# Kernel optimization log

Measured on AMD Instinct MI355X. Metric: run time of the kernel, lower is better.

Reference implementation:

```python
import jax, jax.numpy as jnp
import numpy as np

H0, H1, NL, B, S = 2048, 1024, 8, 2, 2048

def _linear(x, w, b):
    return jnp.einsum('bsd,od->bso', x, w) + b

def setup_inputs() -> dict:
    key = jax.random.key(0)
    ks = jax.random.split(key, 32)
    d = {
        'z':    jax.random.normal(ks[0], (B, S, H0), jnp.float32),
        'act0': jax.random.normal(ks[1], (B, S, H0), jnp.float32),
        'act1': jax.random.normal(ks[2], (B, S, H0), jnp.float32),
        'attmask': jax.random.randint(ks[3], (B, S), 0, 2, jnp.int32),
        'dproj_w': jax.random.normal(ks[4], (H1, H0), jnp.float32) * 0.02,
        'dproj_b': jnp.zeros((H1,), jnp.float32),
        'uproj_w': jax.random.normal(ks[5], (H0, H1), jnp.float32) * 0.02,
        'uproj_b': jnp.zeros((H0,), jnp.float32),
        'wq_w': jax.random.normal(ks[6], (NL, H1, H1), jnp.float32) * 0.02,
        'wq_b': jnp.zeros((NL, H1), jnp.float32),
        'wk_w': jax.random.normal(ks[7], (NL, H1, H1), jnp.float32) * 0.02,
        'wk_b': jnp.zeros((NL, H1), jnp.float32),
        'wv_w': jax.random.normal(ks[8], (NL, H1, H1), jnp.float32) * 0.02,
        'wv_b': jnp.zeros((NL, H1), jnp.float32),
        'mlp1_w': jax.random.normal(ks[9], (NL, 4 * H1, H1), jnp.float32) * 0.02,
        'mlp1_b': jnp.zeros((NL, 4 * H1), jnp.float32),
        'mlp2_w': jax.random.normal(ks[10], (NL, H1, 4 * H1), jnp.float32) * 0.02,
        'mlp2_b': jnp.zeros((NL, H1), jnp.float32),
    }
    return d

def _ladder_fwd(z, act0, act1, attmask, dproj_w, dproj_b, uproj_w, uproj_b,
                wq_w, wq_b, wk_w, wk_b, wv_w, wv_b,
                mlp1_w, mlp1_b, mlp2_w, mlp2_b):
    seq = z.shape[1]
    scale = 1.0 / jnp.sqrt(jnp.float32(H1))
    causal = jnp.tril(jnp.ones((seq, seq), bool))  # [S,S]
    pad = (attmask != 0)[:, None, :]               # [B,1,S] key padding mask
    neg = jnp.float32(-1e9)

    def ladsatt(i, x):
        Q = _linear(x, wq_w[i], wq_b[i])
        K = _linear(x, wk_w[i], wk_b[i])
        V = _linear(x, wv_w[i], wv_b[i])
        scores = jnp.einsum('bqd,bkd->bqk', Q, K) * scale
        scores = jnp.where(causal[None], scores, neg)
        scores = jnp.where(pad, scores, neg)
        w = jax.nn.softmax(scores, axis=-1)
        return jnp.einsum('bqk,bkd->bqd', w, V)

    def mlp(i, x):
        h = jax.nn.relu(_linear(x, mlp1_w[i], mlp1_b[i]))
        return _linear(h, mlp2_w[i], mlp2_b[i])

    rs = _linear(act0, dproj_w, dproj_b)
    rs = rs + ladsatt(0, rs)
    rs = rs + mlp(0, rs)
    rs = rs + _linear(act1, dproj_w, dproj_b)
    rs = rs + ladsatt(1, rs)
    rs = rs + mlp(1, rs)
    for i in range(2, NL):
        rs = rs + ladsatt(i, rs)
        rs = rs + mlp(i, rs)
    return _linear(rs, uproj_w, uproj_b) + z

def reference(z, act0, act1, attmask, dproj_w, dproj_b, uproj_w, uproj_b,
              wq_w, wq_b, wk_w, wk_b, wv_w, wv_b,
              mlp1_w, mlp1_b, mlp2_w, mlp2_b):
    return _ladder_fwd(z, act0, act1, attmask, dproj_w, dproj_b, uproj_w, uproj_b,
                       wq_w, wq_b, wk_w, wk_b, wv_w, wv_b,
                       mlp1_w, mlp1_b, mlp2_w, mlp2_b)
```

## Files before the change

kernel.cpp:

```cpp
#include <hip/hip_runtime.h>
#include <cstdint>


typedef unsigned short u16;
typedef __attribute__((ext_vector_type(8))) __bf16 bf16x8;
typedef __attribute__((ext_vector_type(4))) float f32x4;

#define DI __device__ __forceinline__

constexpr int BB = 2, SSQ = 2048, HH0 = 2048, HH1 = 1024, NLAY = 8, HH4 = 4096;
constexpr int MM = BB * SSQ;

DI float bf2f(u16 h) {
  union { uint32_t u; float f; } x; x.u = ((uint32_t)h) << 16; return x.f;
}
DI u16 f2bf(float f) {
  union { float f; uint32_t u; } x; x.f = f;
  uint32_t u = x.u;
  return (u16)((u + 0x7fffu + ((u >> 16) & 1u)) >> 16);
}

enum {
  FB_BIAS = 1, FB_RES = 2, FB_RELU = 4, FB_F32 = 8, FB_SPLIT = 16,
  FB_CSKIP = 32, FB_CKLOOP = 64
};

template <int F, int KSP>
__global__ __launch_bounds__(256) void gemm_split(
    const u16* __restrict__ Ah, const u16* __restrict__ Al, long sAz, int lda,
    const u16* __restrict__ Bh, const u16* __restrict__ Bl, long sBz, int ldb,
    const float* __restrict__ bias, const float* __restrict__ resF,
    float* Cf, u16* Ch, u16* Cl, long sCz, int ldc, int K, long pstride) {
  int gx = gridDim.x, gy = gridDim.y, gz = gridDim.z;
  long o = blockIdx.x + (long)gx * (blockIdx.y + (long)gy * blockIdx.z);
  long nwg = (long)gx * gy * gz;
  long cq = nwg >> 3, cr = nwg & 7;
  long xcd = o & 7, cidx = o >> 3;
  long sl = (xcd < cr ? xcd * (cq + 1) : cr * (cq + 1) + (xcd - cr) * cq) + cidx;
  int bx = (int)(sl % gx);
  long tt = sl / gx;
  int by = (int)(tt % gy);
  int bzf = (int)(tt / gy);
  int NB = gz / KSP;
  int bz = bzf % NB;
  int ks = bzf / NB;

  if ((F & FB_CSKIP) && bx > by) return;

  __shared__ __align__(16) u16 Ash[128 * 32];
  __shared__ __align__(16) u16 Asl[128 * 32];
  __shared__ __align__(16) u16 Bsh[128 * 32];
  __shared__ __align__(16) u16 Bsl[128 * 32];

  int tid = threadIdx.x;
  int lane = tid & 63;
  int wave = tid >> 6;
  int wr = (wave >> 1) << 6;
  int wc = (wave & 1) << 6;
  int lrow = lane & 15;
  int kg = lane >> 4;
  int kc8 = (kg ^ ((lrow >> 1) & 3)) << 3;

  const u16* Abh = Ah + (long)bz * sAz + ((long)(by << 7)) * lda;
  const u16* Abl = Al + (long)bz * sAz + ((long)(by << 7)) * lda;
  const u16* Bbh = Bh + (long)bz * sBz + ((long)(bx << 7)) * ldb;
  const u16* Bbl = Bl + (long)bz * sBz + ((long)(bx << 7)) * ldb;

  int nKtot = (F & FB_CKLOOP) ? ((by + 1) << 2) : (K >> 5);
  int kbeg = (KSP > 1) ? (ks * nKtot) / KSP : 0;
  int kend = (KSP > 1) ? ((ks + 1) * nKtot) / KSP : nKtot;

  f32x4 acc[4][4] = {};

  for (int kt = kbeg; kt < kend; ++kt) {
    __syncthreads();
    int k0 = kt << 5;
#pragma unroll
    for (int it = 0; it < 2; ++it) {
      int sidx = (it << 8) + tid;
      int r = sidx >> 2;
      int jsw = (sidx & 3) ^ ((r >> 1) & 3);
      long goff = (long)r * lda + (k0 + (jsw << 3));
      long gofB = (long)r * ldb + (k0 + (jsw << 3));
      int loff = sidx << 3;
      __builtin_amdgcn_global_load_lds(
          (__attribute__((address_space(1))) void*)(Abh + goff),
          (__attribute__((address_space(3))) void*)(&Ash[loff]), 16, 0, 0);
      __builtin_amdgcn_global_load_lds(
          (__attribute__((address_space(1))) void*)(Abl + goff),
          (__attribute__((address_space(3))) void*)(&Asl[loff]), 16, 0, 0);
      __builtin_amdgcn_global_load_lds(
          (__attribute__((address_space(1))) void*)(Bbh + gofB),
          (__attribute__((address_space(3))) void*)(&Bsh[loff]), 16, 0, 0);
      __builtin_amdgcn_global_load_lds(
          (__attribute__((address_space(1))) void*)(Bbl + gofB),
          (__attribute__((address_space(3))) void*)(&Bsl[loff]), 16, 0, 0);
    }
    __syncthreads();

    bf16x8 afh[4], bfh[4], bfl[4];
#pragma unroll
    for (int mi = 0; mi < 4; ++mi)
      afh[mi] = *(const bf16x8*)&Ash[((wr + (mi << 4) + lrow) << 5) + kc8];
#pragma unroll
    for (int ni = 0; ni < 4; ++ni) {
      bfh[ni] = *(const bf16x8*)&Bsh[((wc + (ni << 4) + lrow) << 5) + kc8];
      bfl[ni] = *(const bf16x8*)&Bsl[((wc + (ni << 4) + lrow) << 5) + kc8];
    }
#pragma unroll
    for (int mi = 0; mi < 4; ++mi)
#pragma unroll
      for (int ni = 0; ni < 4; ++ni) {
        acc[mi][ni] = __builtin_amdgcn_mfma_f32_16x16x32_bf16(
            afh[mi], bfh[ni], acc[mi][ni], 0, 0, 0);
        acc[mi][ni] = __builtin_amdgcn_mfma_f32_16x16x32_bf16(
            afh[mi], bfl[ni], acc[mi][ni], 0, 0, 0);
      }
    bf16x8 afl[4];
#pragma unroll
    for (int mi = 0; mi < 4; ++mi)
      afl[mi] = *(const bf16x8*)&Asl[((wr + (mi << 4) + lrow) << 5) + kc8];
#pragma unroll
    for (int mi = 0; mi < 4; ++mi)
#pragma unroll
      for (int ni = 0; ni < 4; ++ni)
        acc[mi][ni] = __builtin_amdgcn_mfma_f32_16x16x32_bf16(
            afl[mi], bfh[ni], acc[mi][ni], 0, 0, 0);
  }

  int m0 = (by << 7) + wr + (kg << 2);
  int n0 = (bx << 7) + wc;
#pragma unroll
  for (int mi = 0; mi < 4; ++mi) {
#pragma unroll
    for (int ni = 0; ni < 4; ++ni) {
      int col = n0 + (ni << 4) + lrow;
      float bv = 0.f;
      if ((KSP == 1) && (F & FB_BIAS)) bv = bias[col];
      int rb = m0 + (mi << 4);
#pragma unroll
      for (int r = 0; r < 4; ++r) {
        float v = acc[mi][ni][r];
        long ci = (long)bz * sCz + (long)(rb + r) * ldc + col;
        if constexpr (KSP > 1) {
          Cf[(long)ks * pstride + ci] = v;
        } else {
          v += bv;
          if (F & FB_RELU) v = fmaxf(v, 0.f);
          if (F & FB_RES) v += resF[ci];
          if (F & FB_F32) Cf[ci] = v;
          if (F & FB_SPLIT) {
            u16 h = f2bf(v);
            Ch[ci] = h;
            Cl[ci] = f2bf(v - bf2f(h));
          }
        }
      }
    }
  }
}

template <bool RES>
__global__ void reduce_split(const float* __restrict__ p,
                             const float* __restrict__ bias,
                             float* __restrict__ rs, u16* __restrict__ xh,
                             u16* __restrict__ xl) {
  long i = ((long)blockIdx.x * 256 + threadIdx.x) << 2;
  int col = (int)(i & 1023);
  float4 a = *(const float4*)(p + i);
  float4 b = *(const float4*)(p + i + (long)MM * HH1);
  float4 v;
  v.x = a.x + b.x + bias[col];
  v.y = a.y + b.y + bias[col + 1];
  v.z = a.z + b.z + bias[col + 2];
  v.w = a.w + b.w + bias[col + 3];
  if (RES) {
    float4 r0 = *(const float4*)(rs + i);
    v.x += r0.x; v.y += r0.y; v.z += r0.z; v.w += r0.w;
  }
  *(float4*)(rs + i) = v;
  ushort4 h, l;
  h.x = f2bf(v.x); l.x = f2bf(v.x - bf2f(h.x));
  h.y = f2bf(v.y); l.y = f2bf(v.y - bf2f(h.y));
  h.z = f2bf(v.z); l.z = f2bf(v.z - bf2f(h.z));
  h.w = f2bf(v.w); l.w = f2bf(v.w - bf2f(h.w));
  *(ushort4*)(xh + i) = h;
  *(ushort4*)(xl + i) = l;
}

__global__ void split_kernel(const float* __restrict__ src, u16* __restrict__ hi,
                             u16* __restrict__ lo) {
  long i = ((long)blockIdx.x * 256 + threadIdx.x) << 2;
  float4 v = *(const float4*)(src + i);
  ushort4 h, l;
  h.x = f2bf(v.x); l.x = f2bf(v.x - bf2f(h.x));
  h.y = f2bf(v.y); l.y = f2bf(v.y - bf2f(h.y));
  h.z = f2bf(v.z); l.z = f2bf(v.z - bf2f(h.z));
  h.w = f2bf(v.w); l.w = f2bf(v.w - bf2f(h.w));
  *(ushort4*)(hi + i) = h;
  *(ushort4*)(lo + i) = l;
}

__global__ void concat_bias(const float* __restrict__ qb, const float* __restrict__ kb,
                            const float* __restrict__ vb, float* __restrict__ dst) {
  int j = blockIdx.x * 256 + threadIdx.x;
  float v = (j < 1024) ? qb[j] : ((j < 2048) ? kb[j - 1024] : vb[j - 2048]);
  dst[j] = v;
}

__global__ void deg_kernel(const int* __restrict__ am, int* __restrict__ deg) {
  int i = blockIdx.x * 256 + threadIdx.x;
  int b = i >> 11, q = i & 2047;
  const int* a = am + b * SSQ;
  int any = 0;
  for (int k = 0; k <= q; ++k) any |= (a[k] != 0);
  deg[i] = !any;
}

__global__ void transpose_v(const u16* __restrict__ V, int sld, u16* __restrict__ VT) {
  __shared__ u16 t[64][68];
  int b = blockIdx.z;
  int c0 = blockIdx.x << 6;
  int r0 = blockIdx.y << 6;
  int tr = threadIdx.x >> 4, tc = threadIdx.x & 15;
  const u16* src = V + ((long)(b * SSQ + r0)) * sld + c0;
#pragma unroll
  for (int j = 0; j < 4; ++j) {
    int r = (j << 4) + tr;
    ushort4 u = *(const ushort4*)(src + (long)r * sld + (tc << 2));
    t[r][(tc << 2) + 0] = u.x; t[r][(tc << 2) + 1] = u.y;
    t[r][(tc << 2) + 2] = u.z; t[r][(tc << 2) + 3] = u.w;
  }
  __syncthreads();
  u16* dst = VT + ((long)b * HH1 + c0) * SSQ + r0;
#pragma unroll
  for (int j = 0; j < 4; ++j) {
    int c = (j << 4) + tr;
    ushort4 u;
    u.x = t[(tc << 2) + 0][c]; u.y = t[(tc << 2) + 1][c];
    u.z = t[(tc << 2) + 2][c]; u.w = t[(tc << 2) + 3][c];
    *(ushort4*)(dst + (long)c * SSQ + (tc << 2)) = u;
  }
}

__global__ void colmean_partial(const u16* __restrict__ Vh, const u16* __restrict__ Vl,
                                int ld, float* __restrict__ part) {
  int n = blockIdx.x * 256 + threadIdx.x;
  int b = blockIdx.y, kc = blockIdx.z;
  long base = ((long)(b * SSQ + kc * 256)) * ld + n;
  float s = 0.f;
  for (int k = 0; k < 256; ++k) {
    long o = base + (long)k * ld;
    s += bf2f(Vh[o]) + bf2f(Vl[o]);
  }
  part[((kc * BB) + b) * HH1 + n] = s;
}
__global__ void colmean_final(const float* __restrict__ part, float* __restrict__ mV) {
  int i = blockIdx.x * 256 + threadIdx.x;
  int b = i >> 10, n = i & 1023;
  float s = 0.f;
  for (int kc = 0; kc < 8; ++kc) s += part[((kc * BB) + b) * HH1 + n];
  mV[i] = s * (1.f / (float)SSQ);
}

__global__ void softmax_kernel(const float* __restrict__ sc, u16* __restrict__ Ph,
                               u16* __restrict__ Pl, const int* __restrict__ am,
                               const int* __restrict__ deg) {
  int q = blockIdx.x, b = blockIdx.y;
  int tid = threadIdx.x;
  long rowoff = ((long)b * SSQ + q) * SSQ;
  int qt_end = ((q >> 7) + 1) << 7;
  if (deg[b * SSQ + q]) {
    for (int k = tid; k < qt_end; k += 256) { Ph[rowoff + k] = 0; Pl[rowoff + k] = 0; }
    return;
  }
  const int* a = am + b * SSQ;
  const float scale = 0.03125f;
  constexpr long PSTR = (long)BB * SSQ * SSQ;
  __shared__ float rowbuf[2048];
  __shared__ float sred[8];
  int w = tid >> 6, ln = tid & 63;

  for (int k = tid; k < qt_end; k += 256)
    rowbuf[k] = sc[rowoff + k] + sc[rowoff + k + PSTR];
  __syncthreads();

  float m = -1e30f;
  for (int k = tid; k <= q; k += 256)
    if (a[k]) m = fmaxf(m, rowbuf[k]);
#pragma unroll
  for (int o = 32; o; o >>= 1) m = fmaxf(m, __shfl_xor(m, o));
  if (!ln) sred[w] = m;
  __syncthreads();
  float M = fmaxf(fmaxf(sred[0], sred[1]), fmaxf(sred[2], sred[3]));

  float s = 0.f;
  for (int k = tid; k <= q; k += 256)
    if (a[k]) s += expf((rowbuf[k] - M) * scale);
#pragma unroll
  for (int o = 32; o; o >>= 1) s += __shfl_xor(s, o);
  if (!ln) sred[4 + w] = s;
  __syncthreads();
  float Ssum = sred[4] + sred[5] + sred[6] + sred[7];
  float inv = 1.f / Ssum;

  for (int k = tid; k < qt_end; k += 256) {
    float p = 0.f;
    if (k <= q && a[k]) p = expf((rowbuf[k] - M) * scale) * inv;
    u16 h = f2bf(p);
    Ph[rowoff + k] = h;
    Pl[rowoff + k] = f2bf(p - bf2f(h));
  }
}

__global__ void attn_post(float* __restrict__ rs, const float* __restrict__ pv,
                          u16* __restrict__ xh, u16* __restrict__ xl,
                          const int* __restrict__ deg, const float* __restrict__ mV) {
  long t = (long)blockIdx.x * 256 + threadIdx.x;
  long i = t << 2;
  int row = (int)(i >> 10);
  int col = (int)(i & 1023);
  int b = row >> 11;
  constexpr long PSTR = (long)BB * SSQ * HH1;
  float4 v = *(const float4*)(rs + i);
  float4 a = *(const float4*)(pv + i);
  float4 c = *(const float4*)(pv + i + PSTR);
  v.x += a.x + c.x; v.y += a.y + c.y; v.z += a.z + c.z; v.w += a.w + c.w;
  if (deg[row]) {
    const float* m = mV + (b << 10) + col;
    v.x += m[0]; v.y += m[1]; v.z += m[2]; v.w += m[3];
  }
  *(float4*)(rs + i) = v;
  ushort4 h, l;
  h.x = f2bf(v.x); l.x = f2bf(v.x - bf2f(h.x));
  h.y = f2bf(v.y); l.y = f2bf(v.y - bf2f(h.y));
  h.z = f2bf(v.z); l.z = f2bf(v.z - bf2f(h.z));
  h.w = f2bf(v.w); l.w = f2bf(v.w - bf2f(h.w));
  *(ushort4*)(xh + i) = h;
  *(ushort4*)(xl + i) = l;
}

constexpr size_t MB = 1u << 20;
constexpr size_t OFF_RS    = 0;
constexpr size_t OFF_XH    = 16 * MB;
constexpr size_t OFF_XL    = 24 * MB;
constexpr size_t OFF_QKVH  = 32 * MB;
constexpr size_t OFF_QKVL  = 56 * MB;
constexpr size_t OFF_PH    = 32 * MB;
constexpr size_t OFF_PL    = 48 * MB;
constexpr size_t OFF_RED   = 32 * MB;
constexpr size_t OFF_VTH   = 80 * MB;
constexpr size_t OFF_VTL   = 88 * MB;
constexpr size_t OFF_SC    = 96 * MB;
constexpr size_t OFF_ACTH  = 96 * MB;
constexpr size_t OFF_ACTL  = 112 * MB;
constexpr size_t OFF_HH    = 96 * MB;
constexpr size_t OFF_HL    = 128 * MB;
constexpr size_t OFF_PVP   = 128 * MB;
constexpr size_t OFF_DPWH  = 160 * MB;
constexpr size_t OFF_DPWL  = 164 * MB;
constexpr size_t OFF_UPWH  = 168 * MB;
constexpr size_t OFF_UPWL  = 172 * MB;
constexpr size_t OFF_WQKVH = 176 * MB;
constexpr size_t OFF_WQKVL = 182 * MB;
constexpr size_t OFF_M1H   = 188 * MB;
constexpr size_t OFF_M1L   = 196 * MB;
constexpr size_t OFF_M2H   = 204 * MB;
constexpr size_t OFF_M2L   = 212 * MB;
constexpr size_t OFF_QKVB  = 220 * MB;
constexpr size_t OFF_MV    = OFF_QKVB + 16 * 1024;
constexpr size_t OFF_PART  = OFF_MV + 16 * 1024;
constexpr size_t OFF_DEG   = OFF_PART + 128 * 1024;

extern "C" void kernel_launch(void* const* d_in, const int* in_sizes, int n_in,
                              void* d_out, int out_size, void* d_ws, size_t ws_size,
                              hipStream_t stream) {
  (void)in_sizes; (void)n_in; (void)out_size; (void)ws_size;

  const float* z    = (const float*)d_in[0];
  const float* act0 = (const float*)d_in[1];
  const float* act1 = (const float*)d_in[2];
  const int* amask  = (const int*)d_in[3];
  const float* dpw  = (const float*)d_in[4];
  const float* dpb  = (const float*)d_in[5];
  const float* upw  = (const float*)d_in[6];
  const float* upb  = (const float*)d_in[7];
  const float* wqw  = (const float*)d_in[8];
  const float* wqb  = (const float*)d_in[9];
  const float* wkw  = (const float*)d_in[10];
  const float* wkb  = (const float*)d_in[11];
  const float* wvw  = (const float*)d_in[12];
  const float* wvb  = (const float*)d_in[13];
  const float* m1w  = (const float*)d_in[14];
  const float* m1b  = (const float*)d_in[15];
  const float* m2w  = (const float*)d_in[16];
  const float* m2b  = (const float*)d_in[17];

  char* ws = (char*)d_ws;
  float* rs    = (float*)(ws + OFF_RS);
  u16* xh      = (u16*)(ws + OFF_XH);    u16* xl    = (u16*)(ws + OFF_XL);
  u16* qkvh    = (u16*)(ws + OFF_QKVH);  u16* qkvl  = (u16*)(ws + OFF_QKVL);
  u16* Ph      = (u16*)(ws + OFF_PH);    u16* Pl    = (u16*)(ws + OFF_PL);
  float* redp  = (float*)(ws + OFF_RED);
  u16* VTh     = (u16*)(ws + OFF_VTH);   u16* VTl   = (u16*)(ws + OFF_VTL);
  float* scb   = (float*)(ws + OFF_SC);
  u16* acth    = (u16*)(ws + OFF_ACTH);  u16* actl  = (u16*)(ws + OFF_ACTL);
  u16* hh      = (u16*)(ws + OFF_HH);    u16* hl    = (u16*)(ws + OFF_HL);
  float* pvp   = (float*)(ws + OFF_PVP);
  u16* dpwh    = (u16*)(ws + OFF_DPWH);  u16* dpwl  = (u16*)(ws + OFF_DPWL);
  u16* upwh    = (u16*)(ws + OFF_UPWH);  u16* upwl  = (u16*)(ws + OFF_UPWL);
  u16* wqkvh   = (u16*)(ws + OFF_WQKVH); u16* wqkvl = (u16*)(ws + OFF_WQKVL);
  u16* m1h     = (u16*)(ws + OFF_M1H);   u16* m1l   = (u16*)(ws + OFF_M1L);
  u16* m2h     = (u16*)(ws + OFF_M2H);   u16* m2l   = (u16*)(ws + OFF_M2L);
  float* qkvb  = (float*)(ws + OFF_QKVB);
  float* mV    = (float*)(ws + OFF_MV);
  float* part  = (float*)(ws + OFF_PART);
  int* deg     = (int*)(ws + OFF_DEG);

  deg_kernel<<<dim3((BB * SSQ) / 256), 256, 0, stream>>>(amask, deg);
  split_kernel<<<dim3((HH1 * HH0) / 1024), 256, 0, stream>>>(dpw, dpwh, dpwl);
  split_kernel<<<dim3((HH0 * HH1) / 1024), 256, 0, stream>>>(upw, upwh, upwl);

  split_kernel<<<dim3((MM * HH0) / 1024), 256, 0, stream>>>(act0, acth, actl);
  gemm_split<0, 2><<<dim3(HH1 / 128, MM / 128, 2), 256, 0, stream>>>(
      acth, actl, 0, HH0, dpwh, dpwl, 0, HH0, nullptr, nullptr,
      redp, nullptr, nullptr, 0, HH1, HH0, (long)MM * HH1);
  reduce_split<false><<<dim3(MM * HH1 / 1024), 256, 0, stream>>>(redp, dpb, rs, xh, xl);

  for (int i = 0; i < NLAY; ++i) {
    split_kernel<<<dim3((HH1 * HH1) / 1024), 256, 0, stream>>>(
        wqw + (size_t)i * HH1 * HH1, wqkvh, wqkvl);
    split_kernel<<<dim3((HH1 * HH1) / 1024), 256, 0, stream>>>(
        wkw + (size_t)i * HH1 * HH1, wqkvh + HH1 * HH1, wqkvl + HH1 * HH1);
    split_kernel<<<dim3((HH1 * HH1) / 1024), 256, 0, stream>>>(
        wvw + (size_t)i * HH1 * HH1, wqkvh + 2 * HH1 * HH1, wqkvl + 2 * HH1 * HH1);
    concat_bias<<<dim3(12), 256, 0, stream>>>(wqb + i * HH1, wkb + i * HH1,
                                              wvb + i * HH1, qkvb);
    split_kernel<<<dim3((HH4 * HH1) / 1024), 256, 0, stream>>>(
        m1w + (size_t)i * HH4 * HH1, m1h, m1l);
    split_kernel<<<dim3((HH1 * HH4) / 1024), 256, 0, stream>>>(
        m2w + (size_t)i * HH1 * HH4, m2h, m2l);

    if (i == 1) {
      split_kernel<<<dim3((MM * HH0) / 1024), 256, 0, stream>>>(act1, acth, actl);
      gemm_split<0, 2><<<dim3(HH1 / 128, MM / 128, 2), 256, 0, stream>>>(
          acth, actl, 0, HH0, dpwh, dpwl, 0, HH0, nullptr, nullptr,
          redp, nullptr, nullptr, 0, HH1, HH0, (long)MM * HH1);
      reduce_split<true><<<dim3(MM * HH1 / 1024), 256, 0, stream>>>(redp, dpb, rs, xh, xl);
    }

    gemm_split<FB_BIAS | FB_SPLIT, 1><<<dim3(3072 / 128, MM / 128, 1), 256, 0, stream>>>(
        xh, xl, 0, HH1, wqkvh, wqkvl, 0, HH1, qkvb, nullptr,
        nullptr, qkvh, qkvl, 0, 3072, HH1, 0);

    transpose_v<<<dim3(HH1 / 64, SSQ / 64, BB), 256, 0, stream>>>(qkvh + 2048, 3072, VTh);
    transpose_v<<<dim3(HH1 / 64, SSQ / 64, BB), 256, 0, stream>>>(qkvl + 2048, 3072, VTl);
    colmean_partial<<<dim3(HH1 / 256, BB, 8), 256, 0, stream>>>(
        qkvh + 2048, qkvl + 2048, 3072, part);
    colmean_final<<<dim3((BB * HH1) / 256), 256, 0, stream>>>(part, mV);

    gemm_split<FB_CSKIP, 2><<<dim3(SSQ / 128, SSQ / 128, BB * 2), 256, 0, stream>>>(
        qkvh, qkvl, (long)SSQ * 3072, 3072, qkvh + 1024, qkvl + 1024,
        (long)SSQ * 3072, 3072, nullptr, nullptr,
        scb, nullptr, nullptr, (long)SSQ * SSQ, SSQ, HH1, (long)BB * SSQ * SSQ);

    softmax_kernel<<<dim3(SSQ, BB), 256, 0, stream>>>(scb, Ph, Pl, amask, deg);

    gemm_split<FB_CKLOOP, 2><<<dim3(HH1 / 128, SSQ / 128, BB * 2), 256, 0, stream>>>(
        Ph, Pl, (long)SSQ * SSQ, SSQ, VTh, VTl, (long)HH1 * SSQ, SSQ, nullptr, nullptr,
        pvp, nullptr, nullptr, (long)SSQ * HH1, HH1, SSQ, (long)BB * SSQ * HH1);

    attn_post<<<dim3((MM * HH1 / 4) / 256), 256, 0, stream>>>(rs, pvp, xh, xl, deg, mV);

    gemm_split<FB_BIAS | FB_RELU | FB_SPLIT, 1>
        <<<dim3(HH4 / 128, MM / 128, 1), 256, 0, stream>>>(
        xh, xl, 0, HH1, m1h, m1l, 0, HH1, m1b + i * HH4, nullptr,
        nullptr, hh, hl, 0, HH4, HH1, 0);
    gemm_split<0, 2><<<dim3(HH1 / 128, MM / 128, 2), 256, 0, stream>>>(
        hh, hl, 0, HH4, m2h, m2l, 0, HH4, nullptr, nullptr,
        redp, nullptr, nullptr, 0, HH1, HH4, (long)MM * HH1);
    reduce_split<true><<<dim3(MM * HH1 / 1024), 256, 0, stream>>>(
        redp, m2b + i * HH1, rs, xh, xl);
  }

  gemm_split<FB_BIAS | FB_RES | FB_F32, 1>
      <<<dim3(HH0 / 128, MM / 128, 1), 256, 0, stream>>>(
      xh, xl, 0, HH1, upwh, upwl, 0, HH1, upb, z,
      (float*)d_out, nullptr, nullptr, 0, HH0, HH1, 0);
}
```

Before: 4.406 ms.

## Double-buffer LDS tiles in split-bf16 GEMM to overlap loads with MFMA

Merges the four LDS tile arrays into one two-slot buffer. The loop now issues the direct global-to-LDS loads for tile k+1 before running the MFMA work on tile k. This cuts the barriers per k-step from two to one and aims to hide global load latency behind compute. In exchange, LDS use per block doubles, which lowers how many blocks can run on each CU.

```diff
diff --git a/kernel.cpp b/kernel.cpp
--- a/kernel.cpp
+++ b/kernel.cpp
@@ -47,10 +47,7 @@
 
   if ((F & FB_CSKIP) && bx > by) return;
 
-  __shared__ __align__(16) u16 Ash[128 * 32];
-  __shared__ __align__(16) u16 Asl[128 * 32];
-  __shared__ __align__(16) u16 Bsh[128 * 32];
-  __shared__ __align__(16) u16 Bsl[128 * 32];
+  __shared__ __align__(16) u16 Sbuf[2][4][128 * 32];
 
   int tid = threadIdx.x;
   int lane = tid & 63;
@@ -72,8 +69,7 @@
 
   f32x4 acc[4][4] = {};
 
-  for (int kt = kbeg; kt < kend; ++kt) {
-    __syncthreads();
+  auto STAGE = [&](int buf, int kt) {
     int k0 = kt << 5;
 #pragma unroll
     for (int it = 0; it < 2; ++it) {
@@ -85,27 +81,28 @@
       int loff = sidx << 3;
       __builtin_amdgcn_global_load_lds(
           (__attribute__((address_space(1))) void*)(Abh + goff),
-          (__attribute__((address_space(3))) void*)(&Ash[loff]), 16, 0, 0);
+          (__attribute__((address_space(3))) void*)(&Sbuf[buf][0][loff]), 16, 0, 0);
       __builtin_amdgcn_global_load_lds(
           (__attribute__((address_space(1))) void*)(Abl + goff),
-          (__attribute__((address_space(3))) void*)(&Asl[loff]), 16, 0, 0);
+          (__attribute__((address_space(3))) void*)(&Sbuf[buf][1][loff]), 16, 0, 0);
       __builtin_amdgcn_global_load_lds(
           (__attribute__((address_space(1))) void*)(Bbh + gofB),
-          (__attribute__((address_space(3))) void*)(&Bsh[loff]), 16, 0, 0);
+          (__attribute__((address_space(3))) void*)(&Sbuf[buf][2][loff]), 16, 0, 0);
       __builtin_amdgcn_global_load_lds(
           (__attribute__((address_space(1))) void*)(Bbl + gofB),
-          (__attribute__((address_space(3))) void*)(&Bsl[loff]), 16, 0, 0);
+          (__attribute__((address_space(3))) void*)(&Sbuf[buf][3][loff]), 16, 0, 0);
     }
-    __syncthreads();
-
+  };
+
+  auto COMPUTE = [&](int buf) {
     bf16x8 afh[4], bfh[4], bfl[4];
 #pragma unroll
     for (int mi = 0; mi < 4; ++mi)
-      afh[mi] = *(const bf16x8*)&Ash[((wr + (mi << 4) + lrow) << 5) + kc8];
+      afh[mi] = *(const bf16x8*)&Sbuf[buf][0][((wr + (mi << 4) + lrow) << 5) + kc8];
 #pragma unroll
     for (int ni = 0; ni < 4; ++ni) {
-      bfh[ni] = *(const bf16x8*)&Bsh[((wc + (ni << 4) + lrow) << 5) + kc8];
-      bfl[ni] = *(const bf16x8*)&Bsl[((wc + (ni << 4) + lrow) << 5) + kc8];
+      bfh[ni] = *(const bf16x8*)&Sbuf[buf][2][((wc + (ni << 4) + lrow) << 5) + kc8];
+      bfl[ni] = *(const bf16x8*)&Sbuf[buf][3][((wc + (ni << 4) + lrow) << 5) + kc8];
     }
 #pragma unroll
     for (int mi = 0; mi < 4; ++mi)
@@ -119,14 +116,25 @@
     bf16x8 afl[4];
 #pragma unroll
     for (int mi = 0; mi < 4; ++mi)
-      afl[mi] = *(const bf16x8*)&Asl[((wr + (mi << 4) + lrow) << 5) + kc8];
+      afl[mi] = *(const bf16x8*)&Sbuf[buf][1][((wr + (mi << 4) + lrow) << 5) + kc8];
 #pragma unroll
     for (int mi = 0; mi < 4; ++mi)
 #pragma unroll
       for (int ni = 0; ni < 4; ++ni)
         acc[mi][ni] = __builtin_amdgcn_mfma_f32_16x16x32_bf16(
             afl[mi], bfh[ni], acc[mi][ni], 0, 0, 0);
-  }
+  };
+
+  int cur = 0;
+  STAGE(0, kbeg);
+  __syncthreads();
+  for (int kt = kbeg; kt < kend - 1; ++kt) {
+    STAGE(cur ^ 1, kt + 1);
+    COMPUTE(cur);
+    __syncthreads();
+    cur ^= 1;
+  }
+  COMPUTE(cur);
 
   int m0 = (by << 7) + wr + (kg << 2);
   int n0 = (bx << 7) + wc;
```

After: 4.121 ms. 1.07x faster.
